# Kernel tuning notes

Hardware: AMD Instinct MI355X
Metric: run time of the kernel (lower is better)

Reference implementation:

```python
import jax, jax.numpy as jnp
import numpy as np


def _conv(x, w, b=None, pad=0):
    y = jax.lax.conv_general_dilated(
        x, w, window_strides=(1, 1), padding=[(pad, pad), (pad, pad)],
        dimension_numbers=('NCHW', 'OIHW', 'NCHW'))
    if b is not None:
        y = y + b[None, :, None, None]
    return y


def _resblock(x, w1, w2):
    r = _conv(x, w1, pad=1)
    r = jnp.where(r > 0, r, 0.1 * r)  # LeakyReLU(0.1)
    r = _conv(r, w2, pad=1)
    return r + x


def setup_inputs() -> dict:
    key = jax.random.key(0)
    ks = jax.random.split(key, 8)
    b, c, h, w = 8, 64, 128, 320
    return {
        'x_left': jax.random.normal(ks[0], (b, c, h, w), jnp.float32),
        'x_right': jax.random.normal(ks[1], (b, c, h, w), jnp.float32),
        'rb_w1': jax.random.normal(ks[2], (c, c, 3, 3), jnp.float32) * 0.05,
        'rb_w2': jax.random.normal(ks[3], (c, c, 3, 3), jnp.float32) * 0.05,
        'wl': jax.random.normal(ks[4], (c, c, 1, 1), jnp.float32) * 0.1,
        'bl': jax.random.normal(ks[5], (c,), jnp.float32) * 0.01,
        'wr': jax.random.normal(ks[6], (c, c, 1, 1), jnp.float32) * 0.1,
        'br': jax.random.normal(ks[7], (c,), jnp.float32) * 0.01,
    }


def reference(x_left, x_right, rb_w1, rb_w2, wl, bl, wr, br):
    b, c, h, w = x_left.shape
    buf_l = _resblock(x_left, rb_w1, rb_w2)
    buf_r = _resblock(x_right, rb_w1, rb_w2)
    # 1x1 projections, then per-row attention along width
    F0 = _conv(buf_l, wl, bl).transpose(0, 2, 3, 1)   # (b,h,w,c)
    F1 = _conv(buf_r, wr, br).transpose(0, 2, 3, 1)   # (b,h,w,c)
    S = jnp.einsum('bhwc,bhvc->bhwv', F0, F1)          # (b,h,w,w)
    M_right_to_left = jax.nn.softmax(S, axis=-1)       # (b,h,w,w)
    M_left_to_right = jax.nn.softmax(jnp.swapaxes(S, -1, -2), axis=-1)
    # validity mask: column-sum > 0.1 (detached). skimage morphology (CPU-side) is
    # intentionally omitted; it is outside the GPU kernel scope.
    V = (jnp.sum(jax.lax.stop_gradient(M_left_to_right), axis=2) > 0.1)
    V = V.reshape(b, 1, h, w).astype(jnp.float32)
    # warp right features to left view
    xr = x_right.transpose(0, 2, 3, 1)                 # (b,h,w,c)
    out_f = jnp.einsum('bhwv,bhvc->bhwc', M_right_to_left, xr)
    out_f = out_f.transpose(0, 3, 1, 2)                # (b,c,h,w)
    return (out_f, V,
            (M_left_to_right.reshape(b * h, w, w),
             M_right_to_left.reshape(b * h, w, w)))
```

## Files before the change

### kernel.cpp

```cpp
#include <hip/hip_runtime.h>

#define BB 8
#define CC 64
#define HH 128
#define WW 320

#define N_OUTF (BB*CC*HH*WW)
#define N_V    (BB*HH*WW)
#define N_M    (BB*HH*WW*WW)
#define OFF_V    (N_OUTF)
#define OFF_ML2R (N_OUTF + N_V)
#define OFF_MR2L (OFF_ML2R + N_M)
#define OUT_TOTAL (OFF_MR2L + N_M)
#define WT_FLOATS ((4*36864 + 4*4096)/2)
#define NCL 20971520
#define INV512 (1.f/512.f)

typedef _Float16 half8 __attribute__((ext_vector_type(8)));
typedef _Float16 half4 __attribute__((ext_vector_type(4)));
typedef float f32x4 __attribute__((ext_vector_type(4)));

__global__ __launch_bounds__(256) void k_wt(
    const float* __restrict__ w1, const float* __restrict__ w2,
    const float* __restrict__ wl, const float* __restrict__ wr,
    _Float16* __restrict__ wB1h, _Float16* __restrict__ wB1l,
    _Float16* __restrict__ wB2h, _Float16* __restrict__ wB2l,
    _Float16* __restrict__ wl1h, _Float16* __restrict__ wl1l,
    _Float16* __restrict__ wr1h, _Float16* __restrict__ wr1l)
{
    int tid = blockIdx.x * 256 + threadIdx.x;
    int stride = gridDim.x * 256;
    for (int e = tid; e < 64*9*64; e += stride) {
        int co = e / 576;
        int rem = e - co*576;
        int tap = rem >> 6, ci = rem & 63;
        float v1 = w1[(co*64 + ci)*9 + tap];
        float v2 = w2[(co*64 + ci)*9 + tap];
        _Float16 h1 = (_Float16)v1, h2 = (_Float16)v2;
        wB1h[e] = h1; wB1l[e] = (_Float16)((v1 - (float)h1)*512.f);
        wB2h[e] = h2; wB2l[e] = (_Float16)((v2 - (float)h2)*512.f);
    }
    for (int e = tid; e < 4096; e += stride) {
        float vl = wl[e], vr = wr[e];
        _Float16 hl = (_Float16)vl, hr = (_Float16)vr;
        wl1h[e] = hl; wl1l[e] = (_Float16)((vl - (float)hl)*512.f);
        wr1h[e] = hr; wr1l[e] = (_Float16)((vr - (float)hr)*512.f);
    }
}

__global__ __launch_bounds__(256) void k_conv_a(
    const float* __restrict__ in,
    const _Float16* __restrict__ wBh, const _Float16* __restrict__ wBl,
    _Float16* __restrict__ out_h, _Float16* __restrict__ out_l)
{
    __shared__ __align__(16) char smem[2*3*66*128];
    char* in_sh = smem;
    char* in_sl = smem + 25344;
    const int tid = threadIdx.x;
    const int x0 = blockIdx.x * 64;
    const int y  = blockIdx.y;
    const int b  = blockIdx.z;
    const int lane = tid & 63;
    const int xq = lane & 15, kq = lane >> 4;
    const int n = tid >> 6;

    half8 bwh[18], bwl[18];
    {
        const _Float16* wbh = &wBh[((size_t)(n*16 + xq)*9)*64 + kq*8];
        const _Float16* wbl = &wBl[((size_t)(n*16 + xq)*9)*64 + kq*8];
#pragma unroll
        for (int t = 0; t < 9; ++t)
#pragma unroll
            for (int c = 0; c < 2; ++c) {
                bwh[t*2 + c] = *(const half8*)&wbh[t*64 + c*32];
                bwl[t*2 + c] = *(const half8*)&wbl[t*64 + c*32];
            }
    }

    for (int e = tid; e < 1584; e += 256) {
        int t = e / 66;
        int xx = e - t*66;
        int ry = t >> 3, u = t & 7;
        int gy = y + ry - 1, gx = x0 + xx - 1;
        half8 hh, hl;
#pragma unroll
        for (int j = 0; j < 8; ++j) { hh[j] = (_Float16)0.f; hl[j] = (_Float16)0.f; }
        if ((unsigned)gy < (unsigned)HH && (unsigned)gx < (unsigned)WW) {
            const float* p = &in[((size_t)(b*CC + u*8)*HH + gy)*WW + gx];
#pragma unroll
            for (int j = 0; j < 8; ++j) {
                float v = p[(size_t)j*HH*WW];
                _Float16 h = (_Float16)v;
                hh[j] = h; hl[j] = (_Float16)((v - (float)h)*512.f);
            }
        }
        int off = ((ry*66 + xx)*8 + (u ^ (xx & 7)))*16;
        *(half8*)&in_sh[off] = hh;
        *(half8*)&in_sl[off] = hl;
    }
    __syncthreads();

    f32x4 accm[4], accc[4];
#pragma unroll
    for (int m = 0; m < 4; ++m) { accm[m] = (f32x4)0.f; accc[m] = (f32x4)0.f; }

#pragma unroll
    for (int m = 0; m < 4; ++m) {
        const int xb = m*16 + xq;
#pragma unroll
        for (int t = 0; t < 9; ++t) {
            const int ry = t / 3, kx = t - ry*3;
            const int xxx = xb + kx;
#pragma unroll
            for (int c = 0; c < 2; ++c) {
                const int u = c*4 + kq;
                int off = ((ry*66 + xxx)*8 + (u ^ (xxx & 7)))*16;
                half8 ah = *(const half8*)&in_sh[off];
                half8 al = *(const half8*)&in_sl[off];
                accm[m] = __builtin_amdgcn_mfma_f32_16x16x32_f16(
                    ah, bwh[t*2 + c], accm[m], 0, 0, 0);
                accc[m] = __builtin_amdgcn_mfma_f32_16x16x32_f16(
                    al, bwh[t*2 + c], accc[m], 0, 0, 0);
                accc[m] = __builtin_amdgcn_mfma_f32_16x16x32_f16(
                    ah, bwl[t*2 + c], accc[m], 0, 0, 0);
            }
        }
    }
    __syncthreads();

    char* out_sh = smem;
    char* out_sl = smem + 8192;
#pragma unroll
    for (int m = 0; m < 4; ++m) {
#pragma unroll
        for (int r = 0; r < 4; ++r) {
            int x = m*16 + kq*4 + r;
            int co = n*16 + xq;
            float v = accm[m][r] + accc[m][r]*INV512;
            v = (v > 0.f) ? v : 0.1f*v;
            _Float16 vh = (_Float16)v;
            _Float16 vl = (_Float16)((v - (float)vh)*512.f);
            int boff = (x*8 + ((co >> 3) ^ (x & 7)))*16 + (co & 7)*2;
            *(_Float16*)&out_sh[boff] = vh;
            *(_Float16*)&out_sl[boff] = vl;
        }
    }
    __syncthreads();

#pragma unroll
    for (int i = 0; i < 2; ++i) {
        int unit = tid + 256*i;
        int x = unit >> 3, u = unit & 7;
        int loff = (x*8 + (u ^ (x & 7)))*16;
        size_t g = (((size_t)(b*HH + y)*WW) + x0 + x)*64 + u*8;
        *(half8*)&out_h[g] = *(half8*)&out_sh[loff];
        *(half8*)&out_l[g] = *(half8*)&out_sl[loff];
    }
}

__global__ __launch_bounds__(256) void k_conv_b(
    const _Float16* __restrict__ in_h, const _Float16* __restrict__ in_l,
    const _Float16* __restrict__ wBh, const _Float16* __restrict__ wBl,
    const float* __restrict__ res,
    const _Float16* __restrict__ w1h, const _Float16* __restrict__ w1l,
    const float* __restrict__ bias,
    _Float16* __restrict__ Fh, _Float16* __restrict__ Fl)
{
    __shared__ __align__(16) char smem[2*3*66*128];
    char* in_sh = smem;
    char* in_sl = smem + 25344;
    const int tid = threadIdx.x;
    const int x0 = blockIdx.x * 64;
    const int y  = blockIdx.y;
    const int b  = blockIdx.z;
    const int lane = tid & 63;
    const int xq = lane & 15, kq = lane >> 4;
    const int n = tid >> 6;

    half8 bwh[18], bwl[18];
    {
        const _Float16* wbh = &wBh[((size_t)(n*16 + xq)*9)*64 + kq*8];
        const _Float16* wbl = &wBl[((size_t)(n*16 + xq)*9)*64 + kq*8];
#pragma unroll
        for (int t = 0; t < 9; ++t)
#pragma unroll
            for (int c = 0; c < 2; ++c) {
                bwh[t*2 + c] = *(const half8*)&wbh[t*64 + c*32];
                bwl[t*2 + c] = *(const half8*)&wbl[t*64 + c*32];
            }
    }

    for (int e = tid; e < 3*66*8; e += 256) {
        int ry = e / 528;
        int rem = e - ry*528;
        int xx = rem >> 3, u = rem & 7;
        int gy = y + ry - 1, gx = x0 + xx - 1;
        uint4 vh = make_uint4(0u,0u,0u,0u), vl = make_uint4(0u,0u,0u,0u);
        if ((unsigned)gy < (unsigned)HH && (unsigned)gx < (unsigned)WW) {
            size_t g = (((size_t)(b*HH + gy)*WW) + gx)*64 + u*8;
            vh = *(const uint4*)&in_h[g];
            vl = *(const uint4*)&in_l[g];
        }
        int off = ((ry*66 + xx)*8 + (u ^ (xx & 7)))*16;
        *(uint4*)&in_sh[off] = vh;
        *(uint4*)&in_sl[off] = vl;
    }
    __syncthreads();

    f32x4 accm[4], accc[4];
#pragma unroll
    for (int m = 0; m < 4; ++m) { accm[m] = (f32x4)0.f; accc[m] = (f32x4)0.f; }

#pragma unroll
    for (int m = 0; m < 4; ++m) {
        const int xb = m*16 + xq;
#pragma unroll
        for (int t = 0; t < 9; ++t) {
            const int ry = t / 3, kx = t - ry*3;
            const int xxx = xb + kx;
#pragma unroll
            for (int c = 0; c < 2; ++c) {
                const int u = c*4 + kq;
                int off = ((ry*66 + xxx)*8 + (u ^ (xxx & 7)))*16;
                half8 ah = *(const half8*)&in_sh[off];
                half8 al = *(const half8*)&in_sl[off];
                accm[m] = __builtin_amdgcn_mfma_f32_16x16x32_f16(
                    ah, bwh[t*2 + c], accm[m], 0, 0, 0);
                accc[m] = __builtin_amdgcn_mfma_f32_16x16x32_f16(
                    al, bwh[t*2 + c], accc[m], 0, 0, 0);
                accc[m] = __builtin_amdgcn_mfma_f32_16x16x32_f16(
                    ah, bwl[t*2 + c], accc[m], 0, 0, 0);
            }
        }
    }
    __syncthreads();

    char* out_sh = smem;
    char* out_sl = smem + 8192;
    char* res_sh = smem + 16384;
    char* res_sl = smem + 24576;
    char* w_sh   = smem + 32768;
    char* w_sl   = smem + 40960;

#pragma unroll
    for (int i = 0; i < 2; ++i) {
        int unit = tid + 256*i;
        int x = unit & 63, cu = unit >> 6;
        const float* p = &res[((size_t)(b*CC + cu*8)*HH + y)*WW + x0 + x];
        half8 hh, hl;
#pragma unroll
        for (int j = 0; j < 8; ++j) {
            float v = p[(size_t)j*HH*WW];
            _Float16 h = (_Float16)v;
            hh[j] = h; hl[j] = (_Float16)((v - (float)h)*512.f);
        }
        int off = (x*8 + (cu ^ (x & 7)))*16;
        *(half8*)&res_sh[off] = hh;
        *(half8*)&res_sl[off] = hl;
    }
#pragma unroll
    for (int i = 0; i < 2; ++i) {
        int e = tid + 256*i;
        int co = e >> 3, u = e & 7;
        int off = (co*8 + (u ^ (co & 7)))*16;
        *(half8*)&w_sh[off] = *(const half8*)&w1h[co*64 + u*8];
        *(half8*)&w_sl[off] = *(const half8*)&w1l[co*64 + u*8];
    }
#pragma unroll
    for (int m = 0; m < 4; ++m) {
#pragma unroll
        for (int r = 0; r < 4; ++r) {
            int x = m*16 + kq*4 + r;
            int co = n*16 + xq;
            float v = accm[m][r] + accc[m][r]*INV512;
            _Float16 vh = (_Float16)v;
            _Float16 vl = (_Float16)((v - (float)vh)*512.f);
            int boff = (x*8 + ((co >> 3) ^ (x & 7)))*16 + (co & 7)*2;
            *(_Float16*)&out_sh[boff] = vh;
            *(_Float16*)&out_sl[boff] = vl;
        }
    }
    __syncthreads();

    float bv[4];
#pragma unroll
    for (int nn = 0; nn < 4; ++nn) bv[nn] = bias[nn*16 + (lane & 15)];

    f32x4 am[4], ac[4];
#pragma unroll
    for (int nn = 0; nn < 4; ++nn) { am[nn] = (f32x4)0.f; ac[nn] = (f32x4)0.f; }

    const int arow = (tid >> 6)*16 + (lane & 15);
#pragma unroll
    for (int c = 0; c < 4; ++c) {
        half8 ah, al;
        if (c < 2) {
            int u = c*4 + (lane >> 4);
            int off = (arow*8 + (u ^ (arow & 7)))*16;
            ah = *(const half8*)&out_sh[off];
            al = *(const half8*)&out_sl[off];
        } else {
            int u = (c - 2)*4 + (lane >> 4);
            int off = (arow*8 + (u ^ (arow & 7)))*16;
            ah = *(const half8*)&res_sh[off];
            al = *(const half8*)&res_sl[off];
        }
        int wu = (c & 1)*4 + (lane >> 4);
#pragma unroll
        for (int nn = 0; nn < 4; ++nn) {
            int brow = nn*16 + (lane & 15);
            int woff = (brow*8 + (wu ^ (brow & 7)))*16;
            half8 bh  = *(const half8*)&w_sh[woff];
            half8 blw = *(const half8*)&w_sl[woff];
            am[nn] = __builtin_amdgcn_mfma_f32_16x16x32_f16(ah, bh,  am[nn], 0,0,0);
            ac[nn] = __builtin_amdgcn_mfma_f32_16x16x32_f16(al, bh,  ac[nn], 0,0,0);
            ac[nn] = __builtin_amdgcn_mfma_f32_16x16x32_f16(ah, blw, ac[nn], 0,0,0);
        }
    }
    __syncthreads();

    char* F_sh = smem + 16384;
    char* F_sl = smem + 24576;
#pragma unroll
    for (int nn = 0; nn < 4; ++nn) {
#pragma unroll
        for (int r = 0; r < 4; ++r) {
            int x = (tid >> 6)*16 + (lane >> 4)*4 + r;
            int co = nn*16 + (lane & 15);
            float v = am[nn][r] + ac[nn][r]*INV512 + bv[nn];
            _Float16 vh = (_Float16)v;
            _Float16 vl = (_Float16)((v - (float)vh)*512.f);
            int boff = (x*8 + ((co >> 3) ^ (x & 7)))*16 + (co & 7)*2;
            *(_Float16*)&F_sh[boff] = vh;
            *(_Float16*)&F_sl[boff] = vl;
        }
    }
    __syncthreads();

#pragma unroll
    for (int i = 0; i < 2; ++i) {
        int unit = tid + 256*i;
        int x = unit >> 3, u = unit & 7;
        int loff = (x*8 + (u ^ (x & 7)))*16;
        size_t g = (((size_t)(b*HH + y)*WW) + x0 + x)*64 + u*8;
        *(half8*)&Fh[g] = *(half8*)&F_sh[loff];
        *(half8*)&Fl[g] = *(half8*)&F_sl[loff];
    }
}

__global__ __launch_bounds__(256) void k_sgemm(
    const _Float16* __restrict__ F0h, const _Float16* __restrict__ F0l,
    const _Float16* __restrict__ F1h, const _Float16* __restrict__ F1l,
    float* __restrict__ S,
    float* __restrict__ colmax_p, float* __restrict__ colsum_p,
    float* __restrict__ rowmax_p, float* __restrict__ rowsum_p)
{
    __shared__ __align__(16) char Ah[8192], Al[8192], Bh[8192], Bl[8192];
    __shared__ float cpm[4][64], cpl[4][64];
    const int wt = blockIdx.x, vt = blockIdx.y, row = blockIdx.z;
    const int tid = threadIdx.x, lane = tid & 63, wid = tid >> 6;

    for (int e = tid; e < 512; e += 256) {
        int i = e >> 3, u = e & 7;
        size_t ga = ((size_t)row*WW + wt*64 + i)*64 + u*8;
        size_t gb = ((size_t)row*WW + vt*64 + i)*64 + u*8;
        int off = (i*8 + (u ^ (i & 7)))*16;
        *(uint4*)&Ah[off] = *(const uint4*)&F0h[ga];
        *(uint4*)&Al[off] = *(const uint4*)&F0l[ga];
        *(uint4*)&Bh[off] = *(const uint4*)&F1h[gb];
        *(uint4*)&Bl[off] = *(const uint4*)&F1l[gb];
    }
    __syncthreads();

    f32x4 accm[4], accc[4];
#pragma unroll
    for (int n = 0; n < 4; ++n) { accm[n] = (f32x4)0.f; accc[n] = (f32x4)0.f; }

#pragma unroll
    for (int c = 0; c < 2; ++c) {
        const int u = c*4 + (lane >> 4);
        const int arow = wid*16 + (lane & 15);
        int aoff = (arow*8 + (u ^ (arow & 7)))*16;
        half8 ah = *(const half8*)&Ah[aoff];
        half8 al = *(const half8*)&Al[aoff];
#pragma unroll
        for (int n = 0; n < 4; ++n) {
            const int brow = n*16 + (lane & 15);
            int boff = (brow*8 + (u ^ (brow & 7)))*16;
            half8 bh = *(const half8*)&Bh[boff];
            half8 bl = *(const half8*)&Bl[boff];
            accm[n] = __builtin_amdgcn_mfma_f32_16x16x32_f16(ah, bh, accm[n], 0,0,0);
            accc[n] = __builtin_amdgcn_mfma_f32_16x16x32_f16(al, bh, accc[n], 0,0,0);
            accc[n] = __builtin_amdgcn_mfma_f32_16x16x32_f16(ah, bl, accc[n], 0,0,0);
        }
    }

    float sv[4][4];
#pragma unroll
    for (int n = 0; n < 4; ++n)
#pragma unroll
        for (int r = 0; r < 4; ++r)
            sv[n][r] = accm[n][r] + accc[n][r]*INV512;

#pragma unroll
    for (int n = 0; n < 4; ++n) {
        float* sp = &S[((size_t)row*WW + wt*64 + wid*16 + (lane>>4)*4)*WW
                       + vt*64 + n*16 + (lane & 15)];
#pragma unroll
        for (int r = 0; r < 4; ++r) sp[(size_t)r*WW] = sv[n][r];
    }

    float rmax[4], rsum[4];
#pragma unroll
    for (int r = 0; r < 4; ++r) {
        float m = fmaxf(fmaxf(sv[0][r], sv[1][r]), fmaxf(sv[2][r], sv[3][r]));
        m = fmaxf(m, __shfl_xor(m, 1));
        m = fmaxf(m, __shfl_xor(m, 2));
        m = fmaxf(m, __shfl_xor(m, 4));
        m = fmaxf(m, __shfl_xor(m, 8));
        rmax[r] = m;
        float l = __expf(sv[0][r]-m) + __expf(sv[1][r]-m)
                + __expf(sv[2][r]-m) + __expf(sv[3][r]-m);
        l += __shfl_xor(l, 1); l += __shfl_xor(l, 2);
        l += __shfl_xor(l, 4); l += __shfl_xor(l, 8);
        rsum[r] = l;
    }
    if ((lane & 15) == 0) {
        size_t rbase = ((size_t)row*5 + vt)*WW + wt*64 + wid*16 + (lane>>4)*4;
#pragma unroll
        for (int r = 0; r < 4; ++r) {
            rowmax_p[rbase + r] = rmax[r];
            rowsum_p[rbase + r] = rsum[r];
        }
    }

#pragma unroll
    for (int n = 0; n < 4; ++n) {
        float m = fmaxf(fmaxf(sv[n][0], sv[n][1]), fmaxf(sv[n][2], sv[n][3]));
        m = fmaxf(m, __shfl_xor(m, 16));
        m = fmaxf(m, __shfl_xor(m, 32));
        float l = __expf(sv[n][0]-m) + __expf(sv[n][1]-m)
                + __expf(sv[n][2]-m) + __expf(sv[n][3]-m);
        l += __shfl_xor(l, 16); l += __shfl_xor(l, 32);
        if (lane < 16) { cpm[wid][n*16 + lane] = m; cpl[wid][n*16 + lane] = l; }
    }
    __syncthreads();
    if (tid < 64) {
        float m0 = cpm[0][tid], m1 = cpm[1][tid], m2 = cpm[2][tid], m3 = cpm[3][tid];
        float m = fmaxf(fmaxf(m0, m1), fmaxf(m2, m3));
        float l = cpl[0][tid]*__expf(m0 - m) + cpl[1][tid]*__expf(m1 - m)
                + cpl[2][tid]*__expf(m2 - m) + cpl[3][tid]*__expf(m3 - m);
        size_t cbase = ((size_t)row*5 + wt)*WW + vt*64 + tid;
        colmax_p[cbase] = m;
        colsum_p[cbase] = l;
    }
}

__global__ __launch_bounds__(320) void k_smerge(
    const float* __restrict__ colmax_p, const float* __restrict__ colsum_p,
    const float* __restrict__ rowmax_p, const float* __restrict__ rowsum_p,
    float* __restrict__ colmax_f, float* __restrict__ colinv_f,
    float* __restrict__ rowmax_f, float* __restrict__ rowinv_f)
{
    const int row = blockIdx.x, tid = threadIdx.x;
    float m = -1e30f, l = 0.f;
#pragma unroll
    for (int t = 0; t < 5; ++t) {
        float pm = colmax_p[((size_t)row*5 + t)*WW + tid];
        float pl = colsum_p[((size_t)row*5 + t)*WW + tid];
        float m2 = fmaxf(m, pm);
        l = l*__expf(m - m2) + pl*__expf(pm - m2);
        m = m2;
    }
    colmax_f[(size_t)row*WW + tid] = m;
    colinv_f[(size_t)row*WW + tid] = 1.f/l;
    m = -1e30f; l = 0.f;
#pragma unroll
    for (int t = 0; t < 5; ++t) {
        float pm = rowmax_p[((size_t)row*5 + t)*WW + tid];
        float pl = rowsum_p[((size_t)row*5 + t)*WW + tid];
        float m2 = fmaxf(m, pm);
        l = l*__expf(m - m2) + pl*__expf(pm - m2);
        m = m2;
    }
    rowmax_f[(size_t)row*WW + tid] = m;
    rowinv_f[(size_t)row*WW + tid] = 1.f/l;
}

__global__ __launch_bounds__(256) void k_fused(
    float* __restrict__ S, float* __restrict__ Ml2r, float* __restrict__ Vout,
    const float* __restrict__ xr, float* __restrict__ outf,
    const float* __restrict__ colmax_f, const float* __restrict__ colinv_f,
    const float* __restrict__ rowmax_f, const float* __restrict__ rowinv_f)
{
    __shared__ __align__(16) char A[8192], Bm[8192];
    __shared__ float T[64*65];
    __shared__ float cmx[320], cin[320], rmx[64], rin[64];
    const int wt = blockIdx.x, row = blockIdx.y;
    const int b = row >> 7, h = row & 127;
    const int tid = threadIdx.x, lane = tid & 63, wid = tid >> 6;
    const int wrow = tid >> 2, quad = tid & 3;

    for (int e = tid; e < 320; e += 256) {
        cmx[e] = colmax_f[(size_t)row*WW + e];
        cin[e] = colinv_f[(size_t)row*WW + e];
    }
    if (tid < 64) {
        rmx[tid] = rowmax_f[(size_t)row*WW + wt*64 + tid];
        rin[tid] = rowinv_f[(size_t)row*WW + wt*64 + tid];
    }
    __syncthreads();

    f32x4 acc[4];
#pragma unroll
    for (int n = 0; n < 4; ++n) acc[n] = (f32x4)0.f;
    float vsum = 0.f;
    float* Sbase = &S[((size_t)row*WW + wt*64 + wrow)*WW];
    const float rm = rmx[wrow], ri = rin[wrow];

    for (int vt = 0; vt < 5; ++vt) {
        if (vt) __syncthreads();
#pragma unroll
        for (int i = 0; i < 4; ++i) {
            const int f = quad + 4*i;
            const int v0 = f*4;
            float4 s = *(float4*)&Sbase[vt*64 + v0];
            float4 pr;
            pr.x = __expf(s.x - rm)*ri;
            pr.y = __expf(s.y - rm)*ri;
            pr.z = __expf(s.z - rm)*ri;
            pr.w = __expf(s.w - rm)*ri;
            *(float4*)&Sbase[vt*64 + v0] = pr;
            const int vg = vt*64 + v0;
            float p0 = __expf(s.x - cmx[vg+0])*cin[vg+0];
            float p1 = __expf(s.y - cmx[vg+1])*cin[vg+1];
            float p2 = __expf(s.z - cmx[vg+2])*cin[vg+2];
            float p3 = __expf(s.w - cmx[vg+3])*cin[vg+3];
            T[(v0+0)*65 + wrow] = p0;
            T[(v0+1)*65 + wrow] = p1;
            T[(v0+2)*65 + wrow] = p2;
            T[(v0+3)*65 + wrow] = p3;
            vsum += p0 + p1 + p2 + p3;
            half4 hp;
            hp[0] = (_Float16)pr.x; hp[1] = (_Float16)pr.y;
            hp[2] = (_Float16)pr.z; hp[3] = (_Float16)pr.w;
            *(half4*)&A[(wrow*8 + ((f>>1) ^ (wrow & 7)))*16 + (f & 1)*8] = hp;
        }
        for (int e = tid; e < 512; e += 256) {
            int i = e >> 3, u = e & 7;
            const float4* xp = (const float4*)
                &xr[(((size_t)b*CC + i)*HH + h)*WW + vt*64 + u*8];
            float4 b0 = xp[0], b1 = xp[1];
            half8 hb;
            hb[0]=(_Float16)b0.x; hb[1]=(_Float16)b0.y; hb[2]=(_Float16)b0.z;
            hb[3]=(_Float16)b0.w; hb[4]=(_Float16)b1.x; hb[5]=(_Float16)b1.y;
            hb[6]=(_Float16)b1.z; hb[7]=(_Float16)b1.w;
            *(half8*)&Bm[(i*8 + (u ^ (i & 7)))*16] = hb;
        }
        __syncthreads();
#pragma unroll
        for (int c = 0; c < 2; ++c) {
            const int u = c*4 + (lane >> 4);
            const int arow = wid*16 + (lane & 15);
            half8 ah = *(const half8*)&A[(arow*8 + (u ^ (arow & 7)))*16];
#pragma unroll
            for (int n = 0; n < 4; ++n) {
                const int brow = n*16 + (lane & 15);
                half8 bh = *(const half8*)&Bm[(brow*8 + (u ^ (brow & 7)))*16];
                acc[n] = __builtin_amdgcn_mfma_f32_16x16x32_f16(ah, bh, acc[n], 0,0,0);
            }
        }
        for (int e = tid; e < 4096; e += 256) {
            int vr = e >> 6, wc = e & 63;
            Ml2r[((size_t)row*WW + vt*64 + vr)*WW + wt*64 + wc] = T[vr*65 + wc];
        }
    }

    vsum += __shfl_xor(vsum, 1);
    vsum += __shfl_xor(vsum, 2);
    if (quad == 0)
        Vout[(size_t)row*WW + wt*64 + wrow] = (vsum > 0.1f) ? 1.f : 0.f;

#pragma unroll
    for (int n = 0; n < 4; ++n) {
        *(float4*)&outf[(((size_t)b*CC + n*16 + (lane & 15))*HH + h)*WW
                        + wt*64 + wid*16 + (lane>>4)*4] =
            make_float4(acc[n][0], acc[n][1], acc[n][2], acc[n][3]);
    }
}

__global__ __launch_bounds__(320) void k_softmax(
    float* __restrict__ S, float* __restrict__ Ml2r, float* __restrict__ Vout,
    const float* __restrict__ colmax_f, const float* __restrict__ colinv_f,
    const float* __restrict__ rowmax_f, const float* __restrict__ rowinv_f)
{
    __shared__ float rowmax[320], rowinv[320], colmax[320], colinv[320];
    __shared__ float T[64*65];
    __shared__ float Vp2[5*64];
    const int row = blockIdx.x;
    const int tid = threadIdx.x;
    float* Srow = &S[(size_t)row * WW * WW];

    rowmax[tid] = rowmax_f[(size_t)row*WW + tid];
    rowinv[tid] = rowinv_f[(size_t)row*WW + tid];
    colmax[tid] = colmax_f[(size_t)row*WW + tid];
    colinv[tid] = colinv_f[(size_t)row*WW + tid];
    __syncthreads();

    const int myw = tid & 63;
    const int myg = tid / 64;
    for (int wt = 0; wt < 5; ++wt) {
        float vpart = 0.f;
        for (int vt = 0; vt < 5; ++vt) {
            for (int e = tid; e < 4096; e += 320) {
                int i = e >> 6, j = e & 63;
                int wgl = wt*64 + i, vgl = vt*64 + j;
                size_t si = (size_t)wgl*WW + vgl;
                float s = Srow[si];
                Srow[si] = __expf(s - rowmax[wgl]) * rowinv[wgl];
                T[j*65 + i] = __expf(s - colmax[vgl]) * colinv[vgl];
            }
            __syncthreads();
            for (int e = tid; e < 4096; e += 320) {
                int vr = e >> 6, wc = e & 63;
                Ml2r[((size_t)row*WW + vt*64 + vr)*WW + wt*64 + wc] = T[vr*65 + wc];
            }
            for (int j = myg; j < 64; j += 5) vpart += T[j*65 + myw];
            __syncthreads();
        }
        Vp2[myg*64 + myw] = vpart;
        __syncthreads();
        if (tid < 64) {
            float sv = 0.f;
#pragma unroll
            for (int g = 0; g < 5; ++g) sv += Vp2[g*64 + tid];
            Vout[(size_t)row*WW + wt*64 + tid] = (sv > 0.1f) ? 1.f : 0.f;
        }
        __syncthreads();
    }
}

__global__ __launch_bounds__(256) void k_outgemm(
    const float* __restrict__ M, const float* __restrict__ xr,
    float* __restrict__ outf)
{
    __shared__ __align__(16) char Am[8192], Bm[8192];
    const int wt = blockIdx.x;
    const int row = blockIdx.y;
    const int b = row >> 7, h = row & 127;
    const int tid = threadIdx.x, lane = tid & 63, wid = tid >> 6;

    f32x4 acc[4];
#pragma unroll
    for (int n = 0; n < 4; ++n) acc[n] = (f32x4)0.f;

    for (int vt = 0; vt < 5; ++vt) {
        if (vt) __syncthreads();
        for (int e = tid; e < 512; e += 256) {
            int i = e >> 3, u = e & 7;
            const float4* mp = (const float4*)
                &M[((size_t)row*WW + wt*64 + i)*WW + vt*64 + u*8];
            float4 a0 = mp[0], a1 = mp[1];
            const float4* xp = (const float4*)
                &xr[(((size_t)b*CC + i)*HH + h)*WW + vt*64 + u*8];
            float4 b0 = xp[0], b1 = xp[1];
            half8 ha, hb;
            ha[0]=(_Float16)a0.x; ha[1]=(_Float16)a0.y; ha[2]=(_Float16)a0.z;
            ha[3]=(_Float16)a0.w; ha[4]=(_Float16)a1.x; ha[5]=(_Float16)a1.y;
            ha[6]=(_Float16)a1.z; ha[7]=(_Float16)a1.w;
            hb[0]=(_Float16)b0.x; hb[1]=(_Float16)b0.y; hb[2]=(_Float16)b0.z;
            hb[3]=(_Float16)b0.w; hb[4]=(_Float16)b1.x; hb[5]=(_Float16)b1.y;
            hb[6]=(_Float16)b1.z; hb[7]=(_Float16)b1.w;
            int off = (i*8 + (u ^ (i & 7)))*16;
            *(half8*)&Am[off] = ha;
            *(half8*)&Bm[off] = hb;
        }
        __syncthreads();
#pragma unroll
        for (int c = 0; c < 2; ++c) {
            const int u = c*4 + (lane >> 4);
            const int arow = wid*16 + (lane & 15);
            half8 ah = *(const half8*)&Am[(arow*8 + (u ^ (arow & 7)))*16];
#pragma unroll
            for (int n = 0; n < 4; ++n) {
                const int brow = n*16 + (lane & 15);
                half8 bh = *(const half8*)&Bm[(brow*8 + (u ^ (brow & 7)))*16];
                acc[n] = __builtin_amdgcn_mfma_f32_16x16x32_f16(ah, bh, acc[n], 0,0,0);
            }
        }
    }

#pragma unroll
    for (int n = 0; n < 4; ++n) {
        *(float4*)&outf[(((size_t)b*CC + n*16 + (lane & 15))*HH + h)*WW
                        + wt*64 + wid*16 + (lane>>4)*4] =
            make_float4(acc[n][0], acc[n][1], acc[n][2], acc[n][3]);
    }
}

extern "C" void kernel_launch(void* const* d_in, const int* in_sizes, int n_in,
                              void* d_out, int out_size, void* d_ws, size_t ws_size,
                              hipStream_t stream)
{
    const float* x_l = (const float*)d_in[0];
    const float* x_r = (const float*)d_in[1];
    const float* w1  = (const float*)d_in[2];
    const float* w2  = (const float*)d_in[3];
    const float* wl  = (const float*)d_in[4];
    const float* bl  = (const float*)d_in[5];
    const float* wr  = (const float*)d_in[6];
    const float* br  = (const float*)d_in[7];
    float* out = (float*)d_out;

    float* outf = out;
    float* Vp   = out + OFF_V;
    float* Ml2r = out + OFF_ML2R;
    float* Mr2l = out + OFF_MR2L;

    _Float16* r_h = (_Float16*)Mr2l;
    _Float16* r_l = r_h + (size_t)NCL;
    _Float16* F0h = (_Float16*)Ml2r;
    _Float16* F0l = F0h + (size_t)NCL;
    _Float16* F1h = F0l + (size_t)NCL;
    _Float16* F1l = F1h + (size_t)NCL;
    float* S  = Mr2l;
    _Float16* WTH = (_Float16*)(Ml2r + (size_t)N_M - WT_FLOATS);
    _Float16* wB1h = WTH;
    _Float16* wB1l = WTH + 36864;
    _Float16* wB2h = WTH + 73728;
    _Float16* wB2l = WTH + 110592;
    _Float16* wl1h = WTH + 147456;
    _Float16* wl1l = WTH + 151552;
    _Float16* wr1h = WTH + 155648;
    _Float16* wr1l = WTH + 159744;
    float* colmax_p = out + 0;
    float* colsum_p = out + 1700000;
    float* rowmax_p = out + 3400000;
    float* rowsum_p = out + 5100000;

    const size_t FIN_FLOATS = (size_t)1024*320;
    bool fused = ws_size >= 4*FIN_FLOATS*sizeof(float);
    float* colmax_f, *colinv_f, *rowmax_f, *rowinv_f;
    if (fused) {
        float* ws = (float*)d_ws;
        colmax_f = ws + 0*FIN_FLOATS;
        colinv_f = ws + 1*FIN_FLOATS;
        rowmax_f = ws + 2*FIN_FLOATS;
        rowinv_f = ws + 3*FIN_FLOATS;
    } else {
        colmax_f = out + 6800000;
        colinv_f = out + 7200000;
        rowmax_f = out + 7600000;
        rowinv_f = out + 8000000;
    }

    k_wt<<<64, 256, 0, stream>>>(w1, w2, wl, wr,
                                 wB1h, wB1l, wB2h, wB2l,
                                 wl1h, wl1l, wr1h, wr1l);

    dim3 pgrid(WW/64, HH, BB);
    k_conv_a<<<pgrid, 256, 0, stream>>>(x_l, wB1h, wB1l, r_h, r_l);
    k_conv_b<<<pgrid, 256, 0, stream>>>(r_h, r_l, wB2h, wB2l, x_l,
                                        wl1h, wl1l, bl, F0h, F0l);
    k_conv_a<<<pgrid, 256, 0, stream>>>(x_r, wB1h, wB1l, r_h, r_l);
    k_conv_b<<<pgrid, 256, 0, stream>>>(r_h, r_l, wB2h, wB2l, x_r,
                                        wr1h, wr1l, br, F1h, F1l);

    dim3 sgrid(5, 5, BB*HH);
    k_sgemm<<<sgrid, 256, 0, stream>>>(F0h, F0l, F1h, F1l, S,
                                       colmax_p, colsum_p, rowmax_p, rowsum_p);

    k_smerge<<<BB*HH, 320, 0, stream>>>(colmax_p, colsum_p, rowmax_p, rowsum_p,
                                        colmax_f, colinv_f, rowmax_f, rowinv_f);

    if (fused) {
        dim3 fgrid(5, BB*HH);
        k_fused<<<fgrid, 256, 0, stream>>>(S, Ml2r, Vp, x_r, outf,
                                           colmax_f, colinv_f,
                                           rowmax_f, rowinv_f);
    } else {
        k_softmax<<<BB*HH, 320, 0, stream>>>(S, Ml2r, Vp,
                                             colmax_f, colinv_f,
                                             rowmax_f, rowinv_f);
        dim3 ogrid(5, BB*HH);
        k_outgemm<<<ogrid, 256, 0, stream>>>(Mr2l, x_r, outf);
    }
}
```

Measured before the change: 1.267 ms.

## Retile convs to 2x32 tiles, loop S-gemm over column tiles with online row softmax

Conv kernels now cover two output rows by 32 columns per block instead of one row by 64. The 3x3 halo rows are shared between the two rows, which cuts redundant input loads and shared memory. The S-gemm kernel now loops over all five v-tiles inside one block with double-buffered F1 loads. It keeps an online row max/sum, so the row partials and their merge in k_smerge go away. The Ml2r transpose store is also vectorized to float4, traded against more serial work per block and fewer blocks in the S-gemm grid.

```diff
diff --git a/kernel.cpp b/kernel.cpp
--- a/kernel.cpp
+++ b/kernel.cpp
@@ -53,12 +53,12 @@
     const _Float16* __restrict__ wBh, const _Float16* __restrict__ wBl,
     _Float16* __restrict__ out_h, _Float16* __restrict__ out_l)
 {
-    __shared__ __align__(16) char smem[2*3*66*128];
+    __shared__ __align__(16) char smem[2*4*34*128];
     char* in_sh = smem;
-    char* in_sl = smem + 25344;
+    char* in_sl = smem + 17408;
     const int tid = threadIdx.x;
-    const int x0 = blockIdx.x * 64;
-    const int y  = blockIdx.y;
+    const int x0 = blockIdx.x * 32;
+    const int y0 = blockIdx.y * 2;
     const int b  = blockIdx.z;
     const int lane = tid & 63;
     const int xq = lane & 15, kq = lane >> 4;
@@ -77,11 +77,11 @@
             }
     }
 
-    for (int e = tid; e < 1584; e += 256) {
-        int t = e / 66;
-        int xx = e - t*66;
+    for (int e = tid; e < 1088; e += 256) {
+        int t = e / 34;
+        int xx = e - t*34;
         int ry = t >> 3, u = t & 7;
-        int gy = y + ry - 1, gx = x0 + xx - 1;
+        int gy = y0 + ry - 1, gx = x0 + xx - 1;
         half8 hh, hl;
 #pragma unroll
         for (int j = 0; j < 8; ++j) { hh[j] = (_Float16)0.f; hl[j] = (_Float16)0.f; }
@@ -94,35 +94,41 @@
                 hh[j] = h; hl[j] = (_Float16)((v - (float)h)*512.f);
             }
         }
-        int off = ((ry*66 + xx)*8 + (u ^ (xx & 7)))*16;
+        int off = ((ry*34 + xx)*8 + (u ^ (xx & 7)))*16;
         *(half8*)&in_sh[off] = hh;
         *(half8*)&in_sl[off] = hl;
     }
     __syncthreads();
 
-    f32x4 accm[4], accc[4];
-#pragma unroll
-    for (int m = 0; m < 4; ++m) { accm[m] = (f32x4)0.f; accc[m] = (f32x4)0.f; }
-
-#pragma unroll
-    for (int m = 0; m < 4; ++m) {
-        const int xb = m*16 + xq;
-#pragma unroll
-        for (int t = 0; t < 9; ++t) {
-            const int ry = t / 3, kx = t - ry*3;
-            const int xxx = xb + kx;
-#pragma unroll
-            for (int c = 0; c < 2; ++c) {
-                const int u = c*4 + kq;
-                int off = ((ry*66 + xxx)*8 + (u ^ (xxx & 7)))*16;
-                half8 ah = *(const half8*)&in_sh[off];
-                half8 al = *(const half8*)&in_sl[off];
-                accm[m] = __builtin_amdgcn_mfma_f32_16x16x32_f16(
-                    ah, bwh[t*2 + c], accm[m], 0, 0, 0);
-                accc[m] = __builtin_amdgcn_mfma_f32_16x16x32_f16(
-                    al, bwh[t*2 + c], accc[m], 0, 0, 0);
-                accc[m] = __builtin_amdgcn_mfma_f32_16x16x32_f16(
-                    ah, bwl[t*2 + c], accc[m], 0, 0, 0);
+    f32x4 accm[2][2], accc[2][2];
+#pragma unroll
+    for (int rr = 0; rr < 2; ++rr)
+#pragma unroll
+        for (int m = 0; m < 2; ++m) { accm[rr][m] = (f32x4)0.f; accc[rr][m] = (f32x4)0.f; }
+
+#pragma unroll
+    for (int rr = 0; rr < 2; ++rr) {
+#pragma unroll
+        for (int m = 0; m < 2; ++m) {
+            const int xb = m*16 + xq;
+#pragma unroll
+            for (int t = 0; t < 9; ++t) {
+                const int ry = t / 3, kx = t - ry*3;
+                const int trow = rr + ry;
+                const int xxx = xb + kx;
+#pragma unroll
+                for (int c = 0; c < 2; ++c) {
+                    const int u = c*4 + kq;
+                    int off = ((trow*34 + xxx)*8 + (u ^ (xxx & 7)))*16;
+                    half8 ah = *(const half8*)&in_sh[off];
+                    half8 al = *(const half8*)&in_sl[off];
+                    accm[rr][m] = __builtin_amdgcn_mfma_f32_16x16x32_f16(
+                        ah, bwh[t*2 + c], accm[rr][m], 0, 0, 0);
+                    accc[rr][m] = __builtin_amdgcn_mfma_f32_16x16x32_f16(
+                        al, bwh[t*2 + c], accc[rr][m], 0, 0, 0);
+                    accc[rr][m] = __builtin_amdgcn_mfma_f32_16x16x32_f16(
+                        ah, bwl[t*2 + c], accc[rr][m], 0, 0, 0);
+                }
             }
         }
     }
@@ -131,18 +137,21 @@
     char* out_sh = smem;
     char* out_sl = smem + 8192;
 #pragma unroll
-    for (int m = 0; m < 4; ++m) {
-#pragma unroll
-        for (int r = 0; r < 4; ++r) {
-            int x = m*16 + kq*4 + r;
-            int co = n*16 + xq;
-            float v = accm[m][r] + accc[m][r]*INV512;
-            v = (v > 0.f) ? v : 0.1f*v;
-            _Float16 vh = (_Float16)v;
-            _Float16 vl = (_Float16)((v - (float)vh)*512.f);
-            int boff = (x*8 + ((co >> 3) ^ (x & 7)))*16 + (co & 7)*2;
-            *(_Float16*)&out_sh[boff] = vh;
-            *(_Float16*)&out_sl[boff] = vl;
+    for (int rr = 0; rr < 2; ++rr) {
+#pragma unroll
+        for (int m = 0; m < 2; ++m) {
+#pragma unroll
+            for (int r = 0; r < 4; ++r) {
+                int x = m*16 + kq*4 + r;
+                int co = n*16 + xq;
+                float v = accm[rr][m][r] + accc[rr][m][r]*INV512;
+                v = (v > 0.f) ? v : 0.1f*v;
+                _Float16 vh = (_Float16)v;
+                _Float16 vl = (_Float16)((v - (float)vh)*512.f);
+                int boff = ((rr*32 + x)*8 + ((co >> 3) ^ (x & 7)))*16 + (co & 7)*2;
+                *(_Float16*)&out_sh[boff] = vh;
+                *(_Float16*)&out_sl[boff] = vl;
+            }
         }
     }
     __syncthreads();
@@ -150,9 +159,9 @@
 #pragma unroll
     for (int i = 0; i < 2; ++i) {
         int unit = tid + 256*i;
-        int x = unit >> 3, u = unit & 7;
-        int loff = (x*8 + (u ^ (x & 7)))*16;
-        size_t g = (((size_t)(b*HH + y)*WW) + x0 + x)*64 + u*8;
+        int rr = unit >> 8, x = (unit >> 3) & 31, u = unit & 7;
+        int loff = ((rr*32 + x)*8 + (u ^ (x & 7)))*16;
+        size_t g = (((size_t)(b*HH + y0 + rr)*WW) + x0 + x)*64 + u*8;
         *(half8*)&out_h[g] = *(half8*)&out_sh[loff];
         *(half8*)&out_l[g] = *(half8*)&out_sl[loff];
     }
@@ -166,12 +175,12 @@
     const float* __restrict__ bias,
     _Float16* __restrict__ Fh, _Float16* __restrict__ Fl)
 {
-    __shared__ __align__(16) char smem[2*3*66*128];
+    __shared__ __align__(16) char smem[49152];
     char* in_sh = smem;
-    char* in_sl = smem + 25344;
+    char* in_sl = smem + 17408;
     const int tid = threadIdx.x;
-    const int x0 = blockIdx.x * 64;
-    const int y  = blockIdx.y;
+    const int x0 = blockIdx.x * 32;
+    const int y0 = blockIdx.y * 2;
     const int b  = blockIdx.z;
     const int lane = tid & 63;
     const int xq = lane & 15, kq = lane >> 4;
@@ -190,46 +199,52 @@
             }
     }
 
-    for (int e = tid; e < 3*66*8; e += 256) {
-        int ry = e / 528;
-        int rem = e - ry*528;
-        int xx = rem >> 3, u = rem & 7;
-        int gy = y + ry - 1, gx = x0 + xx - 1;
+    for (int e = tid; e < 1088; e += 256) {
+        int t = e / 34;
+        int xx = e - t*34;
+        int ry = t >> 3, u = t & 7;
+        int gy = y0 + ry - 1, gx = x0 + xx - 1;
         uint4 vh = make_uint4(0u,0u,0u,0u), vl = make_uint4(0u,0u,0u,0u);
         if ((unsigned)gy < (unsigned)HH && (unsigned)gx < (unsigned)WW) {
             size_t g = (((size_t)(b*HH + gy)*WW) + gx)*64 + u*8;
             vh = *(const uint4*)&in_h[g];
             vl = *(const uint4*)&in_l[g];
         }
-        int off = ((ry*66 + xx)*8 + (u ^ (xx & 7)))*16;
+        int off = ((ry*34 + xx)*8 + (u ^ (xx & 7)))*16;
         *(uint4*)&in_sh[off] = vh;
         *(uint4*)&in_sl[off] = vl;
     }
     __syncthreads();
 
-    f32x4 accm[4], accc[4];
-#pragma unroll
-    for (int m = 0; m < 4; ++m) { accm[m] = (f32x4)0.f; accc[m] = (f32x4)0.f; }
-
-#pragma unroll
-    for (int m = 0; m < 4; ++m) {
-        const int xb = m*16 + xq;
-#pragma unroll
-        for (int t = 0; t < 9; ++t) {
-            const int ry = t / 3, kx = t - ry*3;
-            const int xxx = xb + kx;
-#pragma unroll
-            for (int c = 0; c < 2; ++c) {
-                const int u = c*4 + kq;
-                int off = ((ry*66 + xxx)*8 + (u ^ (xxx & 7)))*16;
-                half8 ah = *(const half8*)&in_sh[off];
-                half8 al = *(const half8*)&in_sl[off];
-                accm[m] = __builtin_amdgcn_mfma_f32_16x16x32_f16(
-                    ah, bwh[t*2 + c], accm[m], 0, 0, 0);
-                accc[m] = __builtin_amdgcn_mfma_f32_16x16x32_f16(
-                    al, bwh[t*2 + c], accc[m], 0, 0, 0);
-                accc[m] = __builtin_amdgcn_mfma_f32_16x16x32_f16(
-                    ah, bwl[t*2 + c], accc[m], 0, 0, 0);
+    f32x4 accm[2][2], accc[2][2];
+#pragma unroll
+    for (int rr = 0; rr < 2; ++rr)
+#pragma unroll
+        for (int m = 0; m < 2; ++m) { accm[rr][m] = (f32x4)0.f; accc[rr][m] = (f32x4)0.f; }
+
+#pragma unroll
+    for (int rr = 0; rr < 2; ++rr) {
+#pragma unroll
+        for (int m = 0; m < 2; ++m) {
+            const int xb = m*16 + xq;
+#pragma unroll
+            for (int t = 0; t < 9; ++t) {
+                const int ry = t / 3, kx = t - ry*3;
+                const int trow = rr + ry;
+                const int xxx = xb + kx;
+#pragma unroll
+                for (int c = 0; c < 2; ++c) {
+                    const int u = c*4 + kq;
+                    int off = ((trow*34 + xxx)*8 + (u ^ (xxx & 7)))*16;
+                    half8 ah = *(const half8*)&in_sh[off];
+                    half8 al = *(const half8*)&in_sl[off];
+                    accm[rr][m] = __builtin_amdgcn_mfma_f32_16x16x32_f16(
+                        ah, bwh[t*2 + c], accm[rr][m], 0, 0, 0);
+                    accc[rr][m] = __builtin_amdgcn_mfma_f32_16x16x32_f16(
+                        al, bwh[t*2 + c], accc[rr][m], 0, 0, 0);
+                    accc[rr][m] = __builtin_amdgcn_mfma_f32_16x16x32_f16(
+                        ah, bwl[t*2 + c], accc[rr][m], 0, 0, 0);
+                }
             }
         }
     }
@@ -244,9 +259,9 @@
 
 #pragma unroll
     for (int i = 0; i < 2; ++i) {
-        int unit = tid + 256*i;
-        int x = unit & 63, cu = unit >> 6;
-        const float* p = &res[((size_t)(b*CC + cu*8)*HH + y)*WW + x0 + x];
+        int e = tid + 256*i;
+        int rr = e >> 8, x = (e >> 3) & 31, cu = e & 7;
+        const float* p = &res[((size_t)(b*CC + cu*8)*HH + y0 + rr)*WW + x0 + x];
         half8 hh, hl;
 #pragma unroll
         for (int j = 0; j < 8; ++j) {
@@ -254,7 +269,7 @@
             _Float16 h = (_Float16)v;
             hh[j] = h; hl[j] = (_Float16)((v - (float)h)*512.f);
         }
-        int off = (x*8 + (cu ^ (x & 7)))*16;
+        int off = ((rr*32 + x)*8 + (cu ^ (x & 7)))*16;
         *(half8*)&res_sh[off] = hh;
         *(half8*)&res_sl[off] = hl;
     }
@@ -267,17 +282,20 @@
         *(half8*)&w_sl[off] = *(const half8*)&w1l[co*64 + u*8];
     }
 #pragma unroll
-    for (int m = 0; m < 4; ++m) {
-#pragma unroll
-        for (int r = 0; r < 4; ++r) {
-            int x = m*16 + kq*4 + r;
-            int co = n*16 + xq;
-            float v = accm[m][r] + accc[m][r]*INV512;
-            _Float16 vh = (_Float16)v;
-            _Float16 vl = (_Float16)((v - (float)vh)*512.f);
-            int boff = (x*8 + ((co >> 3) ^ (x & 7)))*16 + (co & 7)*2;
-            *(_Float16*)&out_sh[boff] = vh;
-            *(_Float16*)&out_sl[boff] = vl;
+    for (int rr = 0; rr < 2; ++rr) {
+#pragma unroll
+        for (int m = 0; m < 2; ++m) {
+#pragma unroll
+            for (int r = 0; r < 4; ++r) {
+                int x = m*16 + kq*4 + r;
+                int co = n*16 + xq;
+                float v = accm[rr][m][r] + accc[rr][m][r]*INV512;
+                _Float16 vh = (_Float16)v;
+                _Float16 vl = (_Float16)((v - (float)vh)*512.f);
+                int boff = ((rr*32 + x)*8 + ((co >> 3) ^ (x & 7)))*16 + (co & 7)*2;
+                *(_Float16*)&out_sh[boff] = vh;
+                *(_Float16*)&out_sl[boff] = vl;
+            }
         }
     }
     __syncthreads();
@@ -290,26 +308,23 @@
 #pragma unroll
     for (int nn = 0; nn < 4; ++nn) { am[nn] = (f32x4)0.f; ac[nn] = (f32x4)0.f; }
 
-    const int arow = (tid >> 6)*16 + (lane & 15);
+    const int arow = n*16 + (lane & 15);
 #pragma unroll
     for (int c = 0; c < 4; ++c) {
         half8 ah, al;
+        int u = (c & 1)*4 + (lane >> 4);
+        int off = (arow*8 + (u ^ (arow & 7)))*16;
         if (c < 2) {
-            int u = c*4 + (lane >> 4);
-            int off = (arow*8 + (u ^ (arow & 7)))*16;
             ah = *(const half8*)&out_sh[off];
             al = *(const half8*)&out_sl[off];
         } else {
-            int u = (c - 2)*4 + (lane >> 4);
-            int off = (arow*8 + (u ^ (arow & 7)))*16;
             ah = *(const half8*)&res_sh[off];
             al = *(const half8*)&res_sl[off];
         }
-        int wu = (c & 1)*4 + (lane >> 4);
 #pragma unroll
         for (int nn = 0; nn < 4; ++nn) {
             int brow = nn*16 + (lane & 15);
-            int woff = (brow*8 + (wu ^ (brow & 7)))*16;
+            int woff = (brow*8 + (u ^ (brow & 7)))*16;
             half8 bh  = *(const half8*)&w_sh[woff];
             half8 blw = *(const half8*)&w_sl[woff];
             am[nn] = __builtin_amdgcn_mfma_f32_16x16x32_f16(ah, bh,  am[nn], 0,0,0);
@@ -325,12 +340,12 @@
     for (int nn = 0; nn < 4; ++nn) {
 #pragma unroll
         for (int r = 0; r < 4; ++r) {
-            int x = (tid >> 6)*16 + (lane >> 4)*4 + r;
+            int pos = n*16 + (lane >> 4)*4 + r;
             int co = nn*16 + (lane & 15);
             float v = am[nn][r] + ac[nn][r]*INV512 + bv[nn];
             _Float16 vh = (_Float16)v;
             _Float16 vl = (_Float16)((v - (float)vh)*512.f);
-            int boff = (x*8 + ((co >> 3) ^ (x & 7)))*16 + (co & 7)*2;
+            int boff = (pos*8 + ((co >> 3) ^ (pos & 7)))*16 + (co & 7)*2;
             *(_Float16*)&F_sh[boff] = vh;
             *(_Float16*)&F_sl[boff] = vl;
         }
@@ -340,9 +355,9 @@
 #pragma unroll
     for (int i = 0; i < 2; ++i) {
         int unit = tid + 256*i;
-        int x = unit >> 3, u = unit & 7;
-        int loff = (x*8 + (u ^ (x & 7)))*16;
-        size_t g = (((size_t)(b*HH + y)*WW) + x0 + x)*64 + u*8;
+        int rr = unit >> 8, x = (unit >> 3) & 31, u = unit & 7;
+        int loff = ((rr*32 + x)*8 + (u ^ (x & 7)))*16;
+        size_t g = (((size_t)(b*HH + y0 + rr)*WW) + x0 + x)*64 + u*8;
         *(half8*)&Fh[g] = *(half8*)&F_sh[loff];
         *(half8*)&Fl[g] = *(half8*)&F_sl[loff];
     }
@@ -353,114 +368,159 @@
     const _Float16* __restrict__ F1h, const _Float16* __restrict__ F1l,
     float* __restrict__ S,
     float* __restrict__ colmax_p, float* __restrict__ colsum_p,
-    float* __restrict__ rowmax_p, float* __restrict__ rowsum_p)
+    float* __restrict__ rowmax_f, float* __restrict__ rowinv_f)
 {
-    __shared__ __align__(16) char Ah[8192], Al[8192], Bh[8192], Bl[8192];
-    __shared__ float cpm[4][64], cpl[4][64];
-    const int wt = blockIdx.x, vt = blockIdx.y, row = blockIdx.z;
+    __shared__ __align__(16) char smem[32768];
+    __shared__ float cpm[2][4][64], cpl[2][4][64];
+    const int wt = blockIdx.x, row = blockIdx.y;
     const int tid = threadIdx.x, lane = tid & 63, wid = tid >> 6;
+    char* R0 = smem;
+    char* R1 = smem + 16384;
 
     for (int e = tid; e < 512; e += 256) {
         int i = e >> 3, u = e & 7;
+        int off = (i*8 + (u ^ (i & 7)))*16;
         size_t ga = ((size_t)row*WW + wt*64 + i)*64 + u*8;
-        size_t gb = ((size_t)row*WW + vt*64 + i)*64 + u*8;
-        int off = (i*8 + (u ^ (i & 7)))*16;
-        *(uint4*)&Ah[off] = *(const uint4*)&F0h[ga];
-        *(uint4*)&Al[off] = *(const uint4*)&F0l[ga];
-        *(uint4*)&Bh[off] = *(const uint4*)&F1h[gb];
-        *(uint4*)&Bl[off] = *(const uint4*)&F1l[gb];
-    }
-    __syncthreads();
-
-    f32x4 accm[4], accc[4];
-#pragma unroll
-    for (int n = 0; n < 4; ++n) { accm[n] = (f32x4)0.f; accc[n] = (f32x4)0.f; }
-
-#pragma unroll
-    for (int c = 0; c < 2; ++c) {
-        const int u = c*4 + (lane >> 4);
+        *(uint4*)&R0[off]        = *(const uint4*)&F0h[ga];
+        *(uint4*)&R0[8192 + off] = *(const uint4*)&F0l[ga];
+        size_t gb = ((size_t)row*WW + i)*64 + u*8;
+        *(uint4*)&R1[off]        = *(const uint4*)&F1h[gb];
+        *(uint4*)&R1[8192 + off] = *(const uint4*)&F1l[gb];
+    }
+    __syncthreads();
+
+    half8 ah[2], al[2];
+    {
         const int arow = wid*16 + (lane & 15);
-        int aoff = (arow*8 + (u ^ (arow & 7)))*16;
-        half8 ah = *(const half8*)&Ah[aoff];
-        half8 al = *(const half8*)&Al[aoff];
+#pragma unroll
+        for (int c = 0; c < 2; ++c) {
+            int u = c*4 + (lane >> 4);
+            int aoff = (arow*8 + (u ^ (arow & 7)))*16;
+            ah[c] = *(const half8*)&R0[aoff];
+            al[c] = *(const half8*)&R0[8192 + aoff];
+        }
+    }
+
+    float rm[4], rl[4];
+#pragma unroll
+    for (int r = 0; r < 4; ++r) { rm[r] = -1e30f; rl[r] = 0.f; }
+
+    for (int vt = 0; vt < 5; ++vt) {
+        char* cur = (vt & 1) ? R0 : R1;
+        __syncthreads();
+        if (vt < 4) {
+            char* nxt = (vt & 1) ? R1 : R0;
+            for (int e = tid; e < 512; e += 256) {
+                int i = e >> 3, u = e & 7;
+                int off = (i*8 + (u ^ (i & 7)))*16;
+                size_t gb = ((size_t)row*WW + (vt+1)*64 + i)*64 + u*8;
+                *(uint4*)&nxt[off]        = *(const uint4*)&F1h[gb];
+                *(uint4*)&nxt[8192 + off] = *(const uint4*)&F1l[gb];
+            }
+        }
+        if (vt > 0 && tid < 64) {
+            int pb = (vt-1) & 1;
+            float m0 = cpm[pb][0][tid], m1 = cpm[pb][1][tid];
+            float m2 = cpm[pb][2][tid], m3 = cpm[pb][3][tid];
+            float m = fmaxf(fmaxf(m0, m1), fmaxf(m2, m3));
+            float l = cpl[pb][0][tid]*__expf(m0-m) + cpl[pb][1][tid]*__expf(m1-m)
+                    + cpl[pb][2][tid]*__expf(m2-m) + cpl[pb][3][tid]*__expf(m3-m);
+            size_t cbase = ((size_t)row*5 + wt)*WW + (size_t)(vt-1)*64 + tid;
+            colmax_p[cbase] = m;
+            colsum_p[cbase] = l;
+        }
+
+        f32x4 accm[4], accc[4];
+#pragma unroll
+        for (int n = 0; n < 4; ++n) { accm[n] = (f32x4)0.f; accc[n] = (f32x4)0.f; }
+#pragma unroll
+        for (int c = 0; c < 2; ++c) {
+            const int u = c*4 + (lane >> 4);
+#pragma unroll
+            for (int n = 0; n < 4; ++n) {
+                const int brow = n*16 + (lane & 15);
+                int boff = (brow*8 + (u ^ (brow & 7)))*16;
+                half8 bh = *(const half8*)&cur[boff];
+                half8 bl = *(const half8*)&cur[8192 + boff];
+                accm[n] = __builtin_amdgcn_mfma_f32_16x16x32_f16(ah[c], bh, accm[n], 0,0,0);
+                accc[n] = __builtin_amdgcn_mfma_f32_16x16x32_f16(al[c], bh, accc[n], 0,0,0);
+                accc[n] = __builtin_amdgcn_mfma_f32_16x16x32_f16(ah[c], bl, accc[n], 0,0,0);
+            }
+        }
+
+        float sv[4][4];
+#pragma unroll
+        for (int n = 0; n < 4; ++n)
+#pragma unroll
+            for (int r = 0; r < 4; ++r)
+                sv[n][r] = accm[n][r] + accc[n][r]*INV512;
+
 #pragma unroll
         for (int n = 0; n < 4; ++n) {
-            const int brow = n*16 + (lane & 15);
-            int boff = (brow*8 + (u ^ (brow & 7)))*16;
-            half8 bh = *(const half8*)&Bh[boff];
-            half8 bl = *(const half8*)&Bl[boff];
-            accm[n] = __builtin_amdgcn_mfma_f32_16x16x32_f16(ah, bh, accm[n], 0,0,0);
-            accc[n] = __builtin_amdgcn_mfma_f32_16x16x32_f16(al, bh, accc[n], 0,0,0);
-            accc[n] = __builtin_amdgcn_mfma_f32_16x16x32_f16(ah, bl, accc[n], 0,0,0);
-        }
-    }
-
-    float sv[4][4];
-#pragma unroll
-    for (int n = 0; n < 4; ++n)
-#pragma unroll
-        for (int r = 0; r < 4; ++r)
-            sv[n][r] = accm[n][r] + accc[n][r]*INV512;
-
-#pragma unroll
-    for (int n = 0; n < 4; ++n) {
-        float* sp = &S[((size_t)row*WW + wt*64 + wid*16 + (lane>>4)*4)*WW
-                       + vt*64 + n*16 + (lane & 15)];
-#pragma unroll
-        for (int r = 0; r < 4; ++r) sp[(size_t)r*WW] = sv[n][r];
-    }
-
-    float rmax[4], rsum[4];
-#pragma unroll
-    for (int r = 0; r < 4; ++r) {
-        float m = fmaxf(fmaxf(sv[0][r], sv[1][r]), fmaxf(sv[2][r], sv[3][r]));
-        m = fmaxf(m, __shfl_xor(m, 1));
-        m = fmaxf(m, __shfl_xor(m, 2));
-        m = fmaxf(m, __shfl_xor(m, 4));
-        m = fmaxf(m, __shfl_xor(m, 8));
-        rmax[r] = m;
-        float l = __expf(sv[0][r]-m) + __expf(sv[1][r]-m)
-                + __expf(sv[2][r]-m) + __expf(sv[3][r]-m);
-        l += __shfl_xor(l, 1); l += __shfl_xor(l, 2);
-        l += __shfl_xor(l, 4); l += __shfl_xor(l, 8);
-        rsum[r] = l;
-    }
-    if ((lane & 15) == 0) {
-        size_t rbase = ((size_t)row*5 + vt)*WW + wt*64 + wid*16 + (lane>>4)*4;
+            float* sp = &S[((size_t)row*WW + wt*64 + wid*16 + (lane>>4)*4)*WW
+                           + vt*64 + n*16 + (lane & 15)];
+#pragma unroll
+            for (int r = 0; r < 4; ++r) sp[(size_t)r*WW] = sv[n][r];
+        }
+
 #pragma unroll
         for (int r = 0; r < 4; ++r) {
-            rowmax_p[rbase + r] = rmax[r];
-            rowsum_p[rbase + r] = rsum[r];
-        }
-    }
-
-#pragma unroll
-    for (int n = 0; n < 4; ++n) {
-        float m = fmaxf(fmaxf(sv[n][0], sv[n][1]), fmaxf(sv[n][2], sv[n][3]));
-        m = fmaxf(m, __shfl_xor(m, 16));
-        m = fmaxf(m, __shfl_xor(m, 32));
-        float l = __expf(sv[n][0]-m) + __expf(sv[n][1]-m)
-                + __expf(sv[n][2]-m) + __expf(sv[n][3]-m);
-        l += __shfl_xor(l, 16); l += __shfl_xor(l, 32);
-        if (lane < 16) { cpm[wid][n*16 + lane] = m; cpl[wid][n*16 + lane] = l; }
+            float tmax = fmaxf(fmaxf(sv[0][r], sv[1][r]), fmaxf(sv[2][r], sv[3][r]));
+            float newm = fmaxf(rm[r], tmax);
+            rl[r] = rl[r]*__expf(rm[r] - newm)
+                  + __expf(sv[0][r]-newm) + __expf(sv[1][r]-newm)
+                  + __expf(sv[2][r]-newm) + __expf(sv[3][r]-newm);
+            rm[r] = newm;
+        }
+
+#pragma unroll
+        for (int n = 0; n < 4; ++n) {
+            float m = fmaxf(fmaxf(sv[n][0], sv[n][1]), fmaxf(sv[n][2], sv[n][3]));
+            m = fmaxf(m, __shfl_xor(m, 16));
+            m = fmaxf(m, __shfl_xor(m, 32));
+            float l = __expf(sv[n][0]-m) + __expf(sv[n][1]-m)
+                    + __expf(sv[n][2]-m) + __expf(sv[n][3]-m);
+            l += __shfl_xor(l, 16); l += __shfl_xor(l, 32);
+            if (lane < 16) { cpm[vt&1][wid][n*16 + lane] = m;
+                             cpl[vt&1][wid][n*16 + lane] = l; }
+        }
     }
     __syncthreads();
     if (tid < 64) {
-        float m0 = cpm[0][tid], m1 = cpm[1][tid], m2 = cpm[2][tid], m3 = cpm[3][tid];
+        float m0 = cpm[0][0][tid], m1 = cpm[0][1][tid];
+        float m2 = cpm[0][2][tid], m3 = cpm[0][3][tid];
         float m = fmaxf(fmaxf(m0, m1), fmaxf(m2, m3));
-        float l = cpl[0][tid]*__expf(m0 - m) + cpl[1][tid]*__expf(m1 - m)
-                + cpl[2][tid]*__expf(m2 - m) + cpl[3][tid]*__expf(m3 - m);
-        size_t cbase = ((size_t)row*5 + wt)*WW + vt*64 + tid;
+        float l = cpl[0][0][tid]*__expf(m0-m) + cpl[0][1][tid]*__expf(m1-m)
+                + cpl[0][2][tid]*__expf(m2-m) + cpl[0][3][tid]*__expf(m3-m);
+        size_t cbase = ((size_t)row*5 + wt)*WW + 4*64 + tid;
         colmax_p[cbase] = m;
         colsum_p[cbase] = l;
     }
+
+#pragma unroll
+    for (int r = 0; r < 4; ++r) {
+#pragma unroll
+        for (int o = 1; o < 16; o <<= 1) {
+            float m2 = __shfl_xor(rm[r], o);
+            float l2 = __shfl_xor(rl[r], o);
+            float mm = fmaxf(rm[r], m2);
+            rl[r] = rl[r]*__expf(rm[r] - mm) + l2*__expf(m2 - mm);
+            rm[r] = mm;
+        }
+    }
+    if ((lane & 15) == 0) {
+        size_t rbase = (size_t)row*WW + wt*64 + wid*16 + (lane>>4)*4;
+#pragma unroll
+        for (int r = 0; r < 4; ++r) {
+            rowmax_f[rbase + r] = rm[r];
+            rowinv_f[rbase + r] = 1.f / rl[r];
+        }
+    }
 }
 
 __global__ __launch_bounds__(320) void k_smerge(
     const float* __restrict__ colmax_p, const float* __restrict__ colsum_p,
-    const float* __restrict__ rowmax_p, const float* __restrict__ rowsum_p,
-    float* __restrict__ colmax_f, float* __restrict__ colinv_f,
-    float* __restrict__ rowmax_f, float* __restrict__ rowinv_f)
+    float* __restrict__ colmax_f, float* __restrict__ colinv_f)
 {
     const int row = blockIdx.x, tid = threadIdx.x;
     float m = -1e30f, l = 0.f;
@@ -474,17 +534,6 @@
     }
     colmax_f[(size_t)row*WW + tid] = m;
     colinv_f[(size_t)row*WW + tid] = 1.f/l;
-    m = -1e30f; l = 0.f;
-#pragma unroll
-    for (int t = 0; t < 5; ++t) {
-        float pm = rowmax_p[((size_t)row*5 + t)*WW + tid];
-        float pl = rowsum_p[((size_t)row*5 + t)*WW + tid];
-        float m2 = fmaxf(m, pm);
-        l = l*__expf(m - m2) + pl*__expf(pm - m2);
-        m = m2;
-    }
-    rowmax_f[(size_t)row*WW + tid] = m;
-    rowinv_f[(size_t)row*WW + tid] = 1.f/l;
 }
 
 __global__ __launch_bounds__(256) void k_fused(
@@ -570,9 +619,11 @@
                 acc[n] = __builtin_amdgcn_mfma_f32_16x16x32_f16(ah, bh, acc[n], 0,0,0);
             }
         }
-        for (int e = tid; e < 4096; e += 256) {
-            int vr = e >> 6, wc = e & 63;
-            Ml2r[((size_t)row*WW + vt*64 + vr)*WW + wt*64 + wc] = T[vr*65 + wc];
+        for (int e = tid; e < 1024; e += 256) {
+            int vr = e >> 4, wc4 = (e & 15)*4;
+            const float* tp = &T[vr*65 + wc4];
+            *(float4*)&Ml2r[((size_t)row*WW + vt*64 + vr)*WW + wt*64 + wc4] =
+                make_float4(tp[0], tp[1], tp[2], tp[3]);
         }
     }
 
@@ -735,8 +786,6 @@
     _Float16* wr1l = WTH + 159744;
     float* colmax_p = out + 0;
     float* colsum_p = out + 1700000;
-    float* rowmax_p = out + 3400000;
-    float* rowsum_p = out + 5100000;
 
     const size_t FIN_FLOATS = (size_t)1024*320;
     bool fused = ws_size >= 4*FIN_FLOATS*sizeof(float);
@@ -758,7 +807,7 @@
                                  wB1h, wB1l, wB2h, wB2l,
                                  wl1h, wl1l, wr1h, wr1l);
 
-    dim3 pgrid(WW/64, HH, BB);
+    dim3 pgrid(WW/32, HH/2, BB);
     k_conv_a<<<pgrid, 256, 0, stream>>>(x_l, wB1h, wB1l, r_h, r_l);
     k_conv_b<<<pgrid, 256, 0, stream>>>(r_h, r_l, wB2h, wB2l, x_l,
                                         wl1h, wl1l, bl, F0h, F0l);
@@ -766,12 +815,13 @@
     k_conv_b<<<pgrid, 256, 0, stream>>>(r_h, r_l, wB2h, wB2l, x_r,
                                         wr1h, wr1l, br, F1h, F1l);
 
-    dim3 sgrid(5, 5, BB*HH);
+    dim3 sgrid(5, BB*HH);
     k_sgemm<<<sgrid, 256, 0, stream>>>(F0h, F0l, F1h, F1l, S,
-                                       colmax_p, colsum_p, rowmax_p, rowsum_p);
-
-    k_smerge<<<BB*HH, 320, 0, stream>>>(colmax_p, colsum_p, rowmax_p, rowsum_p,
-                                        colmax_f, colinv_f, rowmax_f, rowinv_f);
+                                       colmax_p, colsum_p,
+                                       rowmax_f, rowinv_f);
+
+    k_smerge<<<BB*HH, 320, 0, stream>>>(colmax_p, colsum_p,
+                                        colmax_f, colinv_f);
 
     if (fused) {
         dim3 fgrid(5, BB*HH);
```

New measurement: 1.166 ms. 1.09x faster.
